# Optimization experiments

Hardware: AMD Instinct MI355X
Metric: run time of the kernel (lower is better)

The kernel has to match this reference:

```python
import jax, jax.numpy as jnp
import numpy as np

B, TQ, TK = 4, 256, 256
Q, K, H = 256, 256, 256


def setup_inputs() -> dict:
    key = jax.random.key(0)
    ks = jax.random.split(key, 10)
    s = 0.05
    return {
        "queries": jax.random.normal(ks[0], (B, TQ, Q), dtype=jnp.float32),
        "keys": jax.random.normal(ks[1], (B, TK, K), dtype=jnp.float32),
        # lengths in [T//2, T] so no fully-masked query rows (torch would NaN there too)
        "query_lengths": jax.random.randint(ks[2], (B,), TQ // 2, TQ + 1),
        "key_lengths": jax.random.randint(ks[3], (B,), TK // 2, TK + 1),
        # nn.Linear(Q+K, H): weight applied as x @ W1; torch concat order is [keys, queries]
        "W1": jax.random.normal(ks[4], (K + Q, H), dtype=jnp.float32) * s,
        "b1": jax.random.normal(ks[5], (H,), dtype=jnp.float32) * s,
        "W2": jax.random.normal(ks[6], (H, H), dtype=jnp.float32) * s,
        "b2": jax.random.normal(ks[7], (H,), dtype=jnp.float32) * s,
        "W3": jax.random.normal(ks[8], (H, 1), dtype=jnp.float32) * s,
        "b3": jax.random.normal(ks[9], (1,), dtype=jnp.float32) * s,
    }


def reference(queries, keys, query_lengths, key_lengths, W1, b1, W2, b2, W3, b3):
    Bn, Tq, Qd = queries.shape
    Tk, Kd = keys.shape[1], keys.shape[2]
    # Split the first linear: concat([keys, queries]) @ W1 == keys@W1[:K] + queries@W1[K:]
    kh = jnp.einsum("bkd,dh->bkh", keys, W1[:Kd])      # [B,Tk,H]
    qh = jnp.einsum("bqd,dh->bqh", queries, W1[Kd:])   # [B,Tq,H]
    h = jax.nn.relu(qh[:, :, None, :] + kh[:, None, :, :] + b1)  # [B,Tq,Tk,H]
    h = jax.nn.relu(jnp.einsum("bqkh,hg->bqkg", h, W2) + b2)     # [B,Tq,Tk,H]
    scores = jnp.einsum("bqkh,h->bqk", h, W3[:, 0]) + b3[0]       # [B,Tq,Tk]
    # mask True where position is padding (query OR key out of range)
    mask = (jnp.arange(Tq)[None, :, None] >= query_lengths[:, None, None]) | (
        jnp.arange(Tk)[None, None, :] >= key_lengths[:, None, None]
    )
    scores = jnp.where(mask, -1e30, scores)
    probs = jax.nn.softmax(scores, axis=-1)
    probs = jnp.where(mask, 0.0, probs)
    return jnp.einsum("bqk,bkd->bqd", probs, keys)  # [B,Tq,K]
```

## Files before the change

### kernel.cpp

```cpp
#include <hip/hip_runtime.h>
#include <cstdint>

#define BATCH 4
#define TQ 256
#define TK 256
#define DIM 256
#define HD 256

typedef _Float16 f16x8 __attribute__((ext_vector_type(8)));
typedef float f32x4 __attribute__((ext_vector_type(4)));

union U4H8 { uint4 u; f16x8 v; };

#define KEEP(x) asm volatile("" : "+v"(x))

__device__ __forceinline__ unsigned short f2h(float f) {
    _Float16 h = (_Float16)f;
    unsigned short u;
    __builtin_memcpy(&u, &h, 2);
    return u;
}

__device__ __forceinline__ uint32_t pk2h(float a, float b) {
    auto r = __builtin_amdgcn_cvt_pkrtz(a, b);
    uint32_t w;
    __builtin_memcpy(&w, &r, 4);
    return w;
}

__global__ __launch_bounds__(256) void prep_all(
    const float* __restrict__ queries, const float* __restrict__ keys,
    const float* __restrict__ W1, const float* __restrict__ b1,
    const float* __restrict__ W2,
    float* __restrict__ qh, float* __restrict__ kh,
    unsigned short* __restrict__ W2T) {
    int i = blockIdx.x;
    int t = threadIdx.x;
    if (i >= 512) {
        __shared__ float tile[32][33];
        int bi = i - 512;
        int tx = t & 31, ty = t >> 5;
        int tc = (bi & 7) * 32, tn = (bi >> 3) * 32;
#pragma unroll
        for (int r = 0; r < 4; ++r)
            tile[ty + r * 8][tx] = W2[(tc + ty + r * 8) * HD + tn + tx];
        __syncthreads();
#pragma unroll
        for (int r = 0; r < 4; ++r)
            W2T[(tn + ty + r * 8) * HD + tc + tx] = f2h(tile[tx][ty + r * 8]);
        return;
    }
    bool isQ = i < 256;
    int r0 = (i & 255) * 4;
    const float* X = isQ ? queries : keys;
    const float* W = W1 + (isQ ? DIM * HD : 0);
    float* O = isQ ? qh : kh;
    __shared__ float xs[4][DIM];
#pragma unroll
    for (int r = 0; r < 4; ++r) xs[r][t] = X[(r0 + r) * DIM + t];
    __syncthreads();
    float acc[4] = {0.f, 0.f, 0.f, 0.f};
#pragma unroll 8
    for (int d = 0; d < DIM; ++d) {
        float w = W[d * HD + t];
#pragma unroll
        for (int r = 0; r < 4; ++r) acc[r] = fmaf(xs[r][d], w, acc[r]);
    }
    float bias = isQ ? b1[t] : 0.f;
#pragma unroll
    for (int r = 0; r < 4; ++r) O[(r0 + r) * HD + t] = acc[r] + bias;
}

__global__ __launch_bounds__(256, 2) void mlp_attn(
    const float* __restrict__ qh, const float* __restrict__ kh,
    const unsigned short* __restrict__ W2T,
    const float* __restrict__ b2, const float* __restrict__ W3,
    const float* __restrict__ keys,
    const int* __restrict__ qlens, const int* __restrict__ klens,
    float* __restrict__ out) {
    int orig = blockIdx.x;
    int bid = ((orig & 7) << 6) | (orig >> 3);
    int b = bid >> 7;
    int q0 = (bid & 127) << 1;
    int t = threadIdx.x;
    int qlen = qlens[b];
    float* orow = out + (b * TQ + q0) * DIM;
    if (q0 >= qlen) { orow[t] = 0.f; orow[DIM + t] = 0.f; return; }
    bool v1 = (q0 + 1) < qlen;
    int klen = klens[b];
    int nch = (klen + 31) >> 5;

    __shared__ uint4 Afrag[2][8][4][64];
    __shared__ float sprt[4][2][TK];
    __shared__ float srow[2][TK];
    __shared__ float red[16];

    int w = t >> 6, lane = t & 63;
    int col = lane & 15, quad = lane >> 4;

    int nb = w << 6;
    uint4 bfr[4][8];
    float b2v[4], w3v[4];
#pragma unroll
    for (int nt = 0; nt < 4; ++nt) {
        int n = nb + (nt << 4) + col;
        const uint4* r = (const uint4*)(W2T + n * HD) + quad;
#pragma unroll
        for (int s = 0; s < 8; ++s) bfr[nt][s] = r[s * 4];
        b2v[nt] = b2[n];
        w3v[nt] = W3[n];
    }

    int rsub = ((w & 1) << 4) | col;
    const float* qrow = qh + (b * TQ + q0 + (w >> 1)) * HD + (quad << 3);
    const float* kbase = kh + b * TK * HD + (quad << 3);

    auto stage = [&](int c, int d) {
        const float* krow = kbase + ((c << 5) + rsub) * HD;
        uint4* as = &Afrag[d][0][w][lane];
#pragma unroll
        for (int s = 0; s < 8; ++s) {
            const float4 k0 = *(const float4*)(krow + s * 32);
            const float4 k1 = *(const float4*)(krow + s * 32 + 4);
            const float4 qa = *(const float4*)(qrow + s * 32);
            const float4 qb = *(const float4*)(qrow + s * 32 + 4);
            uint4 wv;
            wv.x = pk2h(fmaxf(k0.x + qa.x, 0.f), fmaxf(k0.y + qa.y, 0.f));
            wv.y = pk2h(fmaxf(k0.z + qa.z, 0.f), fmaxf(k0.w + qa.w, 0.f));
            wv.z = pk2h(fmaxf(k1.x + qb.x, 0.f), fmaxf(k1.y + qb.y, 0.f));
            wv.w = pk2h(fmaxf(k1.z + qb.z, 0.f), fmaxf(k1.w + qb.w, 0.f));
            as[s * 256] = wv;
        }
    };

    stage(0, 0);

#pragma unroll
    for (int nt = 0; nt < 4; ++nt)
#pragma unroll
        for (int s = 0; s < 8; ++s) {
            KEEP(bfr[nt][s].x); KEEP(bfr[nt][s].y);
            KEEP(bfr[nt][s].z); KEEP(bfr[nt][s].w);
        }

    __syncthreads();

    for (int c = 0; c < nch; ++c) {
        int cur = c & 1;
        if (c + 1 < nch) stage(c + 1, cur ^ 1);

#pragma unroll
        for (int hf = 0; hf < 2; ++hf) {
            f32x4 acc[2][4] = {};
#pragma unroll
            for (int s = 0; s < 8; ++s) {
#pragma unroll
                for (int m2 = 0; m2 < 2; ++m2) {
                    U4H8 au;
                    au.u = Afrag[cur][s][(hf << 1) | m2][lane];
#pragma unroll
                    for (int nt = 0; nt < 4; ++nt) {
                        U4H8 bu;
                        bu.u = bfr[nt][s];
                        acc[m2][nt] = __builtin_amdgcn_mfma_f32_16x16x32_f16(
                            au.v, bu.v, acc[m2][nt], 0, 0, 0);
                    }
                }
            }
#pragma unroll
            for (int m2 = 0; m2 < 2; ++m2) {
                float part[4];
#pragma unroll
                for (int r = 0; r < 4; ++r) {
                    float pa = 0.f;
#pragma unroll
                    for (int nt = 0; nt < 4; ++nt)
                        pa = fmaf(fmaxf(acc[m2][nt][r] + b2v[nt], 0.f), w3v[nt], pa);
                    part[r] = pa;
                }
#pragma unroll
                for (int off = 1; off < 16; off <<= 1)
#pragma unroll
                    for (int r = 0; r < 4; ++r)
                        part[r] += __shfl_xor(part[r], off, 64);
                if (col == 0) {
                    float4 p4 = make_float4(part[0], part[1], part[2], part[3]);
                    *(float4*)&sprt[w][hf][(c << 5) | (m2 << 4) | (quad << 2)] = p4;
                }
            }
        }
        __syncthreads();
    }

    float s0 = -3.4e38f, s1 = -3.4e38f;
    if (t < klen) {
        s0 = (sprt[0][0][t] + sprt[1][0][t]) + (sprt[2][0][t] + sprt[3][0][t]);
        s1 = (sprt[0][1][t] + sprt[1][1][t]) + (sprt[2][1][t] + sprt[3][1][t]);
    }
    float m0 = s0, m1 = s1;
#pragma unroll
    for (int off = 1; off < 64; off <<= 1) {
        m0 = fmaxf(m0, __shfl_xor(m0, off, 64));
        m1 = fmaxf(m1, __shfl_xor(m1, off, 64));
    }
    if (lane == 0) { red[w] = m0; red[8 + w] = m1; }
    __syncthreads();
    m0 = fmaxf(fmaxf(red[0], red[1]), fmaxf(red[2], red[3]));
    m1 = fmaxf(fmaxf(red[8], red[9]), fmaxf(red[10], red[11]));
    float e0 = (t < klen) ? __expf(s0 - m0) : 0.f;
    float e1 = (t < klen) ? __expf(s1 - m1) : 0.f;
    float u0 = e0, u1 = e1;
#pragma unroll
    for (int off = 1; off < 64; off <<= 1) {
        u0 += __shfl_xor(u0, off, 64);
        u1 += __shfl_xor(u1, off, 64);
    }
    if (lane == 0) { red[4 + w] = u0; red[12 + w] = u1; }
    __syncthreads();
    float d0 = red[4] + red[5] + red[6] + red[7];
    float d1 = red[12] + red[13] + red[14] + red[15];
    srow[0][t] = e0 / d0;
    srow[1][t] = e1 / d1;
    __syncthreads();

    float a0 = 0.f, a1 = 0.f;
    const float* kp = keys + b * TK * DIM + t;
#pragma unroll 8
    for (int k = 0; k < klen; ++k) {
        float v = kp[k * DIM];
        a0 = fmaf(srow[0][k], v, a0);
        a1 = fmaf(srow[1][k], v, a1);
    }
    orow[t] = a0;
    orow[DIM + t] = v1 ? a1 : 0.f;
}

extern "C" void kernel_launch(void* const* d_in, const int* in_sizes, int n_in,
                              void* d_out, int out_size, void* d_ws, size_t ws_size,
                              hipStream_t stream) {
    (void)in_sizes; (void)n_in; (void)out_size; (void)ws_size;
    const float* queries = (const float*)d_in[0];
    const float* keys    = (const float*)d_in[1];
    const int*   qlens   = (const int*)d_in[2];
    const int*   klens   = (const int*)d_in[3];
    const float* W1      = (const float*)d_in[4];
    const float* b1      = (const float*)d_in[5];
    const float* W2      = (const float*)d_in[6];
    const float* b2      = (const float*)d_in[7];
    const float* W3      = (const float*)d_in[8];
    float* out = (float*)d_out;

    float* qh = (float*)d_ws;
    float* kh = qh + BATCH * TQ * HD;
    unsigned short* W2T = (unsigned short*)(kh + BATCH * TK * HD);

    prep_all<<<576, 256, 0, stream>>>(queries, keys, W1, b1, W2, qh, kh, W2T);
    mlp_attn<<<BATCH * TQ / 2, 256, 0, stream>>>(
        qh, kh, W2T, b2, W3, keys, qlens, klens, out);
}
```

Baseline: 146.0 us.

## Double mlp_attn block to 512 threads, splitting N tiles across eight waves

The main kernel now runs 8 waves per block instead of 4. Each wave holds half as many W2 column tiles in registers, and staging of the relu(q+k) fragments is split across wave pairs. Per-wave partial scores are now accumulated with shared-memory atomics instead of a 4-way partial buffer. The softmax and the final probs@keys pass are remapped so each of the 512 threads handles one row element and uses float4 key loads with a 4-way k split plus shuffle reduction. The aim is lower register pressure and more latency hiding, at the cost of LDS atomics and non-deterministic summation order. The probs@keys loop now always runs to 256 and relies on probabilities being zeroed past klen.

Result: slower. 172.7 us (+18.3%).

```diff
diff --git a/kernel.cpp b/kernel.cpp
--- a/kernel.cpp
+++ b/kernel.cpp
@@ -71,7 +71,7 @@
     for (int r = 0; r < 4; ++r) O[(r0 + r) * HD + t] = acc[r] + bias;
 }
 
-__global__ __launch_bounds__(256, 2) void mlp_attn(
+__global__ __launch_bounds__(512, 4) void mlp_attn(
     const float* __restrict__ qh, const float* __restrict__ kh,
     const unsigned short* __restrict__ W2T,
     const float* __restrict__ b2, const float* __restrict__ W3,
@@ -85,25 +85,23 @@
     int t = threadIdx.x;
     int qlen = qlens[b];
     float* orow = out + (b * TQ + q0) * DIM;
-    if (q0 >= qlen) { orow[t] = 0.f; orow[DIM + t] = 0.f; return; }
+    if (q0 >= qlen) { orow[t] = 0.f; return; }
     bool v1 = (q0 + 1) < qlen;
     int klen = klens[b];
     int nch = (klen + 31) >> 5;
 
     __shared__ uint4 Afrag[2][8][4][64];
-    __shared__ float sprt[4][2][TK];
     __shared__ float srow[2][TK];
     __shared__ float red[16];
 
     int w = t >> 6, lane = t & 63;
     int col = lane & 15, quad = lane >> 4;
 
-    int nb = w << 6;
-    uint4 bfr[4][8];
-    float b2v[4], w3v[4];
-#pragma unroll
-    for (int nt = 0; nt < 4; ++nt) {
-        int n = nb + (nt << 4) + col;
+    uint4 bfr[2][8];
+    float b2v[2], w3v[2];
+#pragma unroll
+    for (int nt = 0; nt < 2; ++nt) {
+        int n = (w << 5) + (nt << 4) + col;
         const uint4* r = (const uint4*)(W2T + n * HD) + quad;
 #pragma unroll
         for (int s = 0; s < 8; ++s) bfr[nt][s] = r[s * 4];
@@ -111,32 +109,34 @@
         w3v[nt] = W3[n];
     }
 
-    int rsub = ((w & 1) << 4) | col;
-    const float* qrow = qh + (b * TQ + q0 + (w >> 1)) * HD + (quad << 3);
-    const float* kbase = kh + b * TK * HD + (quad << 3);
+    int mt = w >> 1;
+    int sbase = (w & 1) << 2;
+    const float* qrow = qh + (b * TQ + q0 + (mt >> 1)) * HD + (quad << 3) + sbase * 32;
+    const float* kbase = kh + (b * TK + ((mt & 1) << 4) + col) * HD + (quad << 3) + sbase * 32;
 
     auto stage = [&](int c, int d) {
-        const float* krow = kbase + ((c << 5) + rsub) * HD;
-        uint4* as = &Afrag[d][0][w][lane];
-#pragma unroll
-        for (int s = 0; s < 8; ++s) {
-            const float4 k0 = *(const float4*)(krow + s * 32);
-            const float4 k1 = *(const float4*)(krow + s * 32 + 4);
-            const float4 qa = *(const float4*)(qrow + s * 32);
-            const float4 qb = *(const float4*)(qrow + s * 32 + 4);
+        const float* krow = kbase + ((c << 5)) * HD;
+        uint4* as = &Afrag[d][sbase][mt][lane];
+#pragma unroll 2
+        for (int j = 0; j < 4; ++j) {
+            const float4 k0 = *(const float4*)(krow + j * 32);
+            const float4 k1 = *(const float4*)(krow + j * 32 + 4);
+            const float4 qa = *(const float4*)(qrow + j * 32);
+            const float4 qb = *(const float4*)(qrow + j * 32 + 4);
             uint4 wv;
             wv.x = pk2h(fmaxf(k0.x + qa.x, 0.f), fmaxf(k0.y + qa.y, 0.f));
             wv.y = pk2h(fmaxf(k0.z + qa.z, 0.f), fmaxf(k0.w + qa.w, 0.f));
             wv.z = pk2h(fmaxf(k1.x + qb.x, 0.f), fmaxf(k1.y + qb.y, 0.f));
             wv.w = pk2h(fmaxf(k1.z + qb.z, 0.f), fmaxf(k1.w + qb.w, 0.f));
-            as[s * 256] = wv;
+            as[j * 256] = wv;
         }
     };
 
     stage(0, 0);
-
-#pragma unroll
-    for (int nt = 0; nt < 4; ++nt)
+    ((float*)srow)[t] = 0.f;
+
+#pragma unroll
+    for (int nt = 0; nt < 2; ++nt)
 #pragma unroll
         for (int s = 0; s < 8; ++s) {
             KEEP(bfr[nt][s].x); KEEP(bfr[nt][s].y);
@@ -151,7 +151,7 @@
 
 #pragma unroll
         for (int hf = 0; hf < 2; ++hf) {
-            f32x4 acc[2][4] = {};
+            f32x4 acc[2][2] = {};
 #pragma unroll
             for (int s = 0; s < 8; ++s) {
 #pragma unroll
@@ -159,7 +159,7 @@
                     U4H8 au;
                     au.u = Afrag[cur][s][(hf << 1) | m2][lane];
 #pragma unroll
-                    for (int nt = 0; nt < 4; ++nt) {
+                    for (int nt = 0; nt < 2; ++nt) {
                         U4H8 bu;
                         bu.u = bfr[nt][s];
                         acc[m2][nt] = __builtin_amdgcn_mfma_f32_16x16x32_f16(
@@ -172,67 +172,73 @@
                 float part[4];
 #pragma unroll
                 for (int r = 0; r < 4; ++r) {
-                    float pa = 0.f;
-#pragma unroll
-                    for (int nt = 0; nt < 4; ++nt)
-                        pa = fmaf(fmaxf(acc[m2][nt][r] + b2v[nt], 0.f), w3v[nt], pa);
-                    part[r] = pa;
+                    float pa = fmaxf(acc[m2][1][r] + b2v[1], 0.f) * w3v[1];
+                    part[r] = fmaf(fmaxf(acc[m2][0][r] + b2v[0], 0.f), w3v[0], pa);
                 }
 #pragma unroll
                 for (int off = 1; off < 16; off <<= 1)
 #pragma unroll
                     for (int r = 0; r < 4; ++r)
                         part[r] += __shfl_xor(part[r], off, 64);
-                if (col == 0) {
-                    float4 p4 = make_float4(part[0], part[1], part[2], part[3]);
-                    *(float4*)&sprt[w][hf][(c << 5) | (m2 << 4) | (quad << 2)] = p4;
-                }
+                if (col == 0)
+#pragma unroll
+                    for (int r = 0; r < 4; ++r)
+                        atomicAdd(&srow[hf][(c << 5) | (m2 << 4) | (quad << 2) | r],
+                                  part[r]);
             }
         }
         __syncthreads();
     }
 
-    float s0 = -3.4e38f, s1 = -3.4e38f;
-    if (t < klen) {
-        s0 = (sprt[0][0][t] + sprt[1][0][t]) + (sprt[2][0][t] + sprt[3][0][t]);
-        s1 = (sprt[0][1][t] + sprt[1][1][t]) + (sprt[2][1][t] + sprt[3][1][t]);
-    }
-    float m0 = s0, m1 = s1;
-#pragma unroll
-    for (int off = 1; off < 64; off <<= 1) {
-        m0 = fmaxf(m0, __shfl_xor(m0, off, 64));
-        m1 = fmaxf(m1, __shfl_xor(m1, off, 64));
-    }
-    if (lane == 0) { red[w] = m0; red[8 + w] = m1; }
-    __syncthreads();
-    m0 = fmaxf(fmaxf(red[0], red[1]), fmaxf(red[2], red[3]));
-    m1 = fmaxf(fmaxf(red[8], red[9]), fmaxf(red[10], red[11]));
-    float e0 = (t < klen) ? __expf(s0 - m0) : 0.f;
-    float e1 = (t < klen) ? __expf(s1 - m1) : 0.f;
-    float u0 = e0, u1 = e1;
-#pragma unroll
-    for (int off = 1; off < 64; off <<= 1) {
-        u0 += __shfl_xor(u0, off, 64);
-        u1 += __shfl_xor(u1, off, 64);
-    }
-    if (lane == 0) { red[4 + w] = u0; red[12 + w] = u1; }
-    __syncthreads();
-    float d0 = red[4] + red[5] + red[6] + red[7];
-    float d1 = red[12] + red[13] + red[14] + red[15];
-    srow[0][t] = e0 / d0;
-    srow[1][t] = e1 / d1;
-    __syncthreads();
-
-    float a0 = 0.f, a1 = 0.f;
-    const float* kp = keys + b * TK * DIM + t;
+    int rr = t >> 8, kk = t & 255;
+    float s = (kk < klen) ? srow[rr][kk] : -3.4e38f;
+    float m = s;
+#pragma unroll
+    for (int off = 1; off < 64; off <<= 1) m = fmaxf(m, __shfl_xor(m, off, 64));
+    if (lane == 0) red[w] = m;
+    __syncthreads();
+    {
+        int rb = rr << 2;
+        m = fmaxf(fmaxf(red[rb], red[rb + 1]), fmaxf(red[rb + 2], red[rb + 3]));
+    }
+    float e = (kk < klen) ? __expf(s - m) : 0.f;
+    float u = e;
+#pragma unroll
+    for (int off = 1; off < 64; off <<= 1) u += __shfl_xor(u, off, 64);
+    if (lane == 0) red[8 + w] = u;
+    __syncthreads();
+    float denom;
+    {
+        int rb = (rr << 2) + 8;
+        denom = (red[rb] + red[rb + 1]) + (red[rb + 2] + red[rb + 3]);
+    }
+    srow[rr][kk] = e / denom;
+    __syncthreads();
+
+    int cq = (t & 255) >> 2, ks = t & 3;
+    const float* kp = keys + b * TK * DIM + (cq << 2);
+    float4 a = make_float4(0.f, 0.f, 0.f, 0.f);
 #pragma unroll 8
-    for (int k = 0; k < klen; ++k) {
-        float v = kp[k * DIM];
-        a0 = fmaf(srow[0][k], v, a0);
-        a1 = fmaf(srow[1][k], v, a1);
-    }
-    orow[t] = a0;
-    orow[DIM + t] = v1 ? a1 : 0.f;
+    for (int i = 0; i < 64; ++i) {
+        int k = (i << 2) | ks;
+        float p = srow[rr][k];
+        const float4 kv = *(const float4*)(kp + k * DIM);
+        a.x = fmaf(p, kv.x, a.x);
+        a.y = fmaf(p, kv.y, a.y);
+        a.z = fmaf(p, kv.z, a.z);
+        a.w = fmaf(p, kv.w, a.w);
+    }
+#pragma unroll
+    for (int off = 1; off <= 2; off <<= 1) {
+        a.x += __shfl_xor(a.x, off, 64);
+        a.y += __shfl_xor(a.y, off, 64);
+        a.z += __shfl_xor(a.z, off, 64);
+        a.w += __shfl_xor(a.w, off, 64);
+    }
+    if (ks == 0) {
+        float4 o = (rr == 1 && !v1) ? make_float4(0.f, 0.f, 0.f, 0.f) : a;
+        *(float4*)(orow + rr * DIM + (cq << 2)) = o;
+    }
 }
 
 extern "C" void kernel_launch(void* const* d_in, const int* in_sizes, int n_in,
@@ -255,6 +261,6 @@
     unsigned short* W2T = (unsigned short*)(kh + BATCH * TK * HD);
 
     prep_all<<<576, 256, 0, stream>>>(queries, keys, W1, b1, W2, qh, kh, W2T);
-    mlp_attn<<<BATCH * TQ / 2, 256, 0, stream>>>(
+    mlp_attn<<<BATCH * TQ / 2, 512, 0, stream>>>(
         qh, kh, W2T, b2, W3, keys, qlens, klens, out);
 }
```

## Interleave next-chunk kh loads and staging with MFMA tiles, cache q rows in LDS

Applied to the files above, without the earlier changes.

The per-chunk loop is restructured so that the global kh loads and the A-fragment staging for the next chunk are split into pieces. These pieces are interleaved between the MFMA m-tiles and epilogues, with sched_barriers fixing the order. Query hidden rows are copied once into LDS and read from there instead of from global memory on every stage. The aim is to hide global load latency behind matrix work, at the cost of more live registers and smaller accumulator tiles, which may reduce MFMA batching.

New measurement: 134.7 us. 7.7% less time.

```diff
diff --git a/kernel.cpp b/kernel.cpp
--- a/kernel.cpp
+++ b/kernel.cpp
@@ -93,6 +93,7 @@
     __shared__ uint4 Afrag[2][8][4][64];
     __shared__ float sprt[4][2][TK];
     __shared__ float srow[2][TK];
+    __shared__ float Qlds[2][HD];
     __shared__ float red[16];
 
     int w = t >> 6, lane = t & 63;
@@ -111,19 +112,20 @@
         w3v[nt] = W3[n];
     }
 
+    int qsel = w >> 1;
     int rsub = ((w & 1) << 4) | col;
-    const float* qrow = qh + (b * TQ + q0 + (w >> 1)) * HD + (quad << 3);
-    const float* kbase = kh + b * TK * HD + (quad << 3);
-
-    auto stage = [&](int c, int d) {
-        const float* krow = kbase + ((c << 5) + rsub) * HD;
-        uint4* as = &Afrag[d][0][w][lane];
+    const float* kbase = kh + (b * TK + rsub) * HD + (quad << 3);
+
+    {
+        const float* qrowg = qh + (b * TQ + q0 + qsel) * HD + (quad << 3);
+        const float* krow = kbase;
+        uint4* as = &Afrag[0][0][w][lane];
 #pragma unroll
         for (int s = 0; s < 8; ++s) {
             const float4 k0 = *(const float4*)(krow + s * 32);
             const float4 k1 = *(const float4*)(krow + s * 32 + 4);
-            const float4 qa = *(const float4*)(qrow + s * 32);
-            const float4 qb = *(const float4*)(qrow + s * 32 + 4);
+            const float4 qa = *(const float4*)(qrowg + s * 32);
+            const float4 qb = *(const float4*)(qrowg + s * 32 + 4);
             uint4 wv;
             wv.x = pk2h(fmaxf(k0.x + qa.x, 0.f), fmaxf(k0.y + qa.y, 0.f));
             wv.y = pk2h(fmaxf(k0.z + qa.z, 0.f), fmaxf(k0.w + qa.w, 0.f));
@@ -131,9 +133,9 @@
             wv.w = pk2h(fmaxf(k1.z + qb.z, 0.f), fmaxf(k1.w + qb.w, 0.f));
             as[s * 256] = wv;
         }
-    };
-
-    stage(0, 0);
+    }
+    Qlds[0][t] = qh[(b * TQ + q0) * HD + t];
+    Qlds[1][t] = qh[(b * TQ + q0 + 1) * HD + t];
 
 #pragma unroll
     for (int nt = 0; nt < 4; ++nt)
@@ -145,49 +147,103 @@
 
     __syncthreads();
 
+    auto sloop = [&](int cur, int mt, f32x4* acc) {
+#pragma unroll
+        for (int s = 0; s < 8; ++s) {
+            U4H8 au;
+            au.u = Afrag[cur][s][mt][lane];
+#pragma unroll
+            for (int nt = 0; nt < 4; ++nt) {
+                U4H8 bu;
+                bu.u = bfr[nt][s];
+                acc[nt] = __builtin_amdgcn_mfma_f32_16x16x32_f16(
+                    au.v, bu.v, acc[nt], 0, 0, 0);
+            }
+        }
+    };
+    auto epi = [&](int c, int mt, const f32x4* acc) {
+        int hf = mt >> 1, m2 = mt & 1;
+        float part[4];
+#pragma unroll
+        for (int r = 0; r < 4; ++r) {
+            float pa = 0.f;
+#pragma unroll
+            for (int nt = 0; nt < 4; ++nt)
+                pa = fmaf(fmaxf(acc[nt][r] + b2v[nt], 0.f), w3v[nt], pa);
+            part[r] = pa;
+        }
+#pragma unroll
+        for (int off = 1; off < 16; off <<= 1)
+#pragma unroll
+            for (int r = 0; r < 4; ++r)
+                part[r] += __shfl_xor(part[r], off, 64);
+        if (col == 0)
+            *(float4*)&sprt[w][hf][(c << 5) | (m2 << 4) | (quad << 2)] =
+                make_float4(part[0], part[1], part[2], part[3]);
+    };
+
     for (int c = 0; c < nch; ++c) {
         int cur = c & 1;
-        if (c + 1 < nch) stage(c + 1, cur ^ 1);
-
-#pragma unroll
-        for (int hf = 0; hf < 2; ++hf) {
-            f32x4 acc[2][4] = {};
-#pragma unroll
-            for (int s = 0; s < 8; ++s) {
-#pragma unroll
-                for (int m2 = 0; m2 < 2; ++m2) {
-                    U4H8 au;
-                    au.u = Afrag[cur][s][(hf << 1) | m2][lane];
-#pragma unroll
-                    for (int nt = 0; nt < 4; ++nt) {
-                        U4H8 bu;
-                        bu.u = bfr[nt][s];
-                        acc[m2][nt] = __builtin_amdgcn_mfma_f32_16x16x32_f16(
-                            au.v, bu.v, acc[m2][nt], 0, 0, 0);
-                    }
-                }
+        bool stg = (c + 1 < nch);
+        const float* krow = kbase + (((c + 1) << 5)) * HD;
+        uint4* as1 = &Afrag[cur ^ 1][0][w][lane];
+
+        auto wslot = [&](int s, const float4& k0, const float4& k1) {
+            const float4 qa = *(const float4*)&Qlds[qsel][s * 32 + (quad << 3)];
+            const float4 qb = *(const float4*)&Qlds[qsel][s * 32 + (quad << 3) + 4];
+            uint4 wv;
+            wv.x = pk2h(fmaxf(k0.x + qa.x, 0.f), fmaxf(k0.y + qa.y, 0.f));
+            wv.y = pk2h(fmaxf(k0.z + qa.z, 0.f), fmaxf(k0.w + qa.w, 0.f));
+            wv.z = pk2h(fmaxf(k1.x + qb.x, 0.f), fmaxf(k1.y + qb.y, 0.f));
+            wv.w = pk2h(fmaxf(k1.z + qb.z, 0.f), fmaxf(k1.w + qb.w, 0.f));
+            as1[s * 256] = wv;
+        };
+
+        float4 A0, A1, A2, A3, B0, B1, B2, B3;
+        if (stg) {
+            A0 = *(const float4*)(krow);       A1 = *(const float4*)(krow + 4);
+            A2 = *(const float4*)(krow + 32);  A3 = *(const float4*)(krow + 36);
+        }
+        __builtin_amdgcn_sched_barrier(0);
+
+        {
+            f32x4 acc[4] = {};
+            sloop(cur, 0, acc);
+            if (stg) {
+                wslot(0, A0, A1); wslot(1, A2, A3);
+                B0 = *(const float4*)(krow + 64);  B1 = *(const float4*)(krow + 68);
+                B2 = *(const float4*)(krow + 96);  B3 = *(const float4*)(krow + 100);
             }
-#pragma unroll
-            for (int m2 = 0; m2 < 2; ++m2) {
-                float part[4];
-#pragma unroll
-                for (int r = 0; r < 4; ++r) {
-                    float pa = 0.f;
-#pragma unroll
-                    for (int nt = 0; nt < 4; ++nt)
-                        pa = fmaf(fmaxf(acc[m2][nt][r] + b2v[nt], 0.f), w3v[nt], pa);
-                    part[r] = pa;
-                }
-#pragma unroll
-                for (int off = 1; off < 16; off <<= 1)
-#pragma unroll
-                    for (int r = 0; r < 4; ++r)
-                        part[r] += __shfl_xor(part[r], off, 64);
-                if (col == 0) {
-                    float4 p4 = make_float4(part[0], part[1], part[2], part[3]);
-                    *(float4*)&sprt[w][hf][(c << 5) | (m2 << 4) | (quad << 2)] = p4;
-                }
+            __builtin_amdgcn_sched_barrier(0);
+            epi(c, 0, acc);
+            if (stg) {
+                wslot(2, B0, B1); wslot(3, B2, B3);
+                A0 = *(const float4*)(krow + 128); A1 = *(const float4*)(krow + 132);
+                A2 = *(const float4*)(krow + 160); A3 = *(const float4*)(krow + 164);
             }
+            __builtin_amdgcn_sched_barrier(0);
+        }
+        {
+            f32x4 acc[4] = {};
+            sloop(cur, 1, acc);
+            if (stg) {
+                wslot(4, A0, A1); wslot(5, A2, A3);
+                B0 = *(const float4*)(krow + 192); B1 = *(const float4*)(krow + 196);
+                B2 = *(const float4*)(krow + 224); B3 = *(const float4*)(krow + 228);
+            }
+            __builtin_amdgcn_sched_barrier(0);
+            epi(c, 1, acc);
+            if (stg) { wslot(6, B0, B1); wslot(7, B2, B3); }
+        }
+        {
+            f32x4 acc[4] = {};
+            sloop(cur, 2, acc);
+            epi(c, 2, acc);
+        }
+        {
+            f32x4 acc[4] = {};
+            sloop(cur, 3, acc);
+            epi(c, 3, acc);
         }
         __syncthreads();
     }
```

## Store fp16 projections, stage key tiles via direct LDS loads, 4 queries per block

Applied to the files above, without the earlier changes.

The prep kernel now writes qh and kh as fp16, with an XOR swizzle applied to the kh rows. The main kernel uses 512-thread blocks that each handle 4 query rows and 64-key chunks. Key tiles are streamed into LDS with global_load_lds, and the fp16 add+ReLU is done in registers right before the MFMA, with W2 fragments held as the A operand. This cuts global traffic for kh and reuses each key tile across 4 queries, but it needs more LDS, uses fp16 accumulation for the hidden pre-activation, and adds s_setprio hints.

Result: slower. 149.4 us (+2.4%).

```diff
diff --git a/kernel.cpp b/kernel.cpp
--- a/kernel.cpp
+++ b/kernel.cpp
@@ -21,18 +21,22 @@
     return u;
 }
 
-__device__ __forceinline__ uint32_t pk2h(float a, float b) {
-    auto r = __builtin_amdgcn_cvt_pkrtz(a, b);
-    uint32_t w;
-    __builtin_memcpy(&w, &r, 4);
-    return w;
+__device__ __forceinline__ f16x8 relu8(f16x8 h) {
+    f16x8 z = {};
+#if __has_builtin(__builtin_elementwise_max)
+    return __builtin_elementwise_max(h, z);
+#else
+#pragma unroll
+    for (int i = 0; i < 8; ++i) h[i] = h[i] > (_Float16)0 ? h[i] : (_Float16)0;
+    return h;
+#endif
 }
 
 __global__ __launch_bounds__(256) void prep_all(
     const float* __restrict__ queries, const float* __restrict__ keys,
     const float* __restrict__ W1, const float* __restrict__ b1,
     const float* __restrict__ W2,
-    float* __restrict__ qh, float* __restrict__ kh,
+    unsigned short* __restrict__ qhh, unsigned short* __restrict__ khh,
     unsigned short* __restrict__ W2T) {
     int i = blockIdx.x;
     int t = threadIdx.x;
@@ -54,7 +58,6 @@
     int r0 = (i & 255) * 4;
     const float* X = isQ ? queries : keys;
     const float* W = W1 + (isQ ? DIM * HD : 0);
-    float* O = isQ ? qh : kh;
     __shared__ float xs[4][DIM];
 #pragma unroll
     for (int r = 0; r < 4; ++r) xs[r][t] = X[(r0 + r) * DIM + t];
@@ -66,81 +69,85 @@
 #pragma unroll
         for (int r = 0; r < 4; ++r) acc[r] = fmaf(xs[r][d], w, acc[r]);
     }
-    float bias = isQ ? b1[t] : 0.f;
-#pragma unroll
-    for (int r = 0; r < 4; ++r) O[(r0 + r) * HD + t] = acc[r] + bias;
-}
-
-__global__ __launch_bounds__(256, 2) void mlp_attn(
-    const float* __restrict__ qh, const float* __restrict__ kh,
+    if (isQ) {
+        float bias = b1[t];
+#pragma unroll
+        for (int r = 0; r < 4; ++r) qhh[(r0 + r) * HD + t] = f2h(acc[r] + bias);
+    } else {
+#pragma unroll
+        for (int r = 0; r < 4; ++r) {
+            int rr = r0 + r;
+            khh[rr * HD + (t ^ ((rr & 7) << 3))] = f2h(acc[r]);
+        }
+    }
+}
+
+__global__ __launch_bounds__(512, 2) void mlp_attn(
+    const unsigned short* __restrict__ khh,
+    const unsigned short* __restrict__ qhh,
     const unsigned short* __restrict__ W2T,
     const float* __restrict__ b2, const float* __restrict__ W3,
     const float* __restrict__ keys,
     const int* __restrict__ qlens, const int* __restrict__ klens,
     float* __restrict__ out) {
     int orig = blockIdx.x;
-    int bid = ((orig & 7) << 6) | (orig >> 3);
-    int b = bid >> 7;
-    int q0 = (bid & 127) << 1;
+    int bid = ((orig & 7) << 5) | (orig >> 3);
+    int b = bid >> 6;
+    int q0 = (bid & 63) << 2;
     int t = threadIdx.x;
     int qlen = qlens[b];
-    float* orow = out + (b * TQ + q0) * DIM;
-    if (q0 >= qlen) { orow[t] = 0.f; orow[DIM + t] = 0.f; return; }
-    bool v1 = (q0 + 1) < qlen;
+    float* obase = out + (b * TQ + q0) * DIM;
+    if (q0 >= qlen) { obase[t] = 0.f; obase[512 + t] = 0.f; return; }
     int klen = klens[b];
-    int nch = (klen + 31) >> 5;
-
-    __shared__ uint4 Afrag[2][8][4][64];
-    __shared__ float sprt[4][2][TK];
-    __shared__ float srow[2][TK];
-    __shared__ float red[16];
+    int nch = (klen + 63) >> 6;
+
+    __shared__ unsigned short khbuf[2][64 * HD];
+    __shared__ unsigned short qbuf[4][HD];
+    __shared__ float sprt[8][4][TK];
+    __shared__ float pbuf[4][TK];
+    __shared__ float red[32];
 
     int w = t >> 6, lane = t & 63;
     int col = lane & 15, quad = lane >> 4;
 
-    int nb = w << 6;
-    uint4 bfr[4][8];
-    float b2v[4], w3v[4];
-#pragma unroll
-    for (int nt = 0; nt < 4; ++nt) {
-        int n = nb + (nt << 4) + col;
+    auto stage = [&](int c, int d) {
+        const char* src = (const char*)(khh + ((size_t)b * TK + (c << 6)) * HD) + t * 16;
+        char* dst = (char*)&khbuf[d][0] + t * 16;
+#pragma unroll
+        for (int i = 0; i < 4; ++i)
+            __builtin_amdgcn_global_load_lds((const uint32_t*)(src + i * 8192),
+                                             (uint32_t*)(dst + i * 8192), 16, 0, 0);
+    };
+    stage(0, 0);
+
+    uint4 afr[2][8];
+#pragma unroll
+    for (int nt = 0; nt < 2; ++nt) {
+        int n = (w << 5) + (nt << 4) + col;
         const uint4* r = (const uint4*)(W2T + n * HD) + quad;
 #pragma unroll
-        for (int s = 0; s < 8; ++s) bfr[nt][s] = r[s * 4];
-        b2v[nt] = b2[n];
-        w3v[nt] = W3[n];
-    }
-
-    int rsub = ((w & 1) << 4) | col;
-    const float* qrow = qh + (b * TQ + q0 + (w >> 1)) * HD + (quad << 3);
-    const float* kbase = kh + b * TK * HD + (quad << 3);
-
-    auto stage = [&](int c, int d) {
-        const float* krow = kbase + ((c << 5) + rsub) * HD;
-        uint4* as = &Afrag[d][0][w][lane];
+        for (int s = 0; s < 8; ++s) afr[nt][s] = r[s * 4];
+    }
+    float b2v[2][4], w3v[2][4];
+#pragma unroll
+    for (int nt = 0; nt < 2; ++nt)
+#pragma unroll
+        for (int r = 0; r < 4; ++r) {
+            int n = (w << 5) + (nt << 4) + (quad << 2) + r;
+            b2v[nt][r] = b2[n];
+            w3v[nt][r] = W3[n];
+        }
+
+    if (t < 128)
+        *(uint4*)((char*)&qbuf[0][0] + t * 16) =
+            *(const uint4*)((const char*)(qhh + ((size_t)b * TQ + q0) * HD) + t * 16);
+
+#pragma unroll
+    for (int nt = 0; nt < 2; ++nt)
 #pragma unroll
         for (int s = 0; s < 8; ++s) {
-            const float4 k0 = *(const float4*)(krow + s * 32);
-            const float4 k1 = *(const float4*)(krow + s * 32 + 4);
-            const float4 qa = *(const float4*)(qrow + s * 32);
-            const float4 qb = *(const float4*)(qrow + s * 32 + 4);
-            uint4 wv;
-            wv.x = pk2h(fmaxf(k0.x + qa.x, 0.f), fmaxf(k0.y + qa.y, 0.f));
-            wv.y = pk2h(fmaxf(k0.z + qa.z, 0.f), fmaxf(k0.w + qa.w, 0.f));
-            wv.z = pk2h(fmaxf(k1.x + qb.x, 0.f), fmaxf(k1.y + qb.y, 0.f));
-            wv.w = pk2h(fmaxf(k1.z + qb.z, 0.f), fmaxf(k1.w + qb.w, 0.f));
-            as[s * 256] = wv;
-        }
-    };
-
-    stage(0, 0);
-
-#pragma unroll
-    for (int nt = 0; nt < 4; ++nt)
-#pragma unroll
-        for (int s = 0; s < 8; ++s) {
-            KEEP(bfr[nt][s].x); KEEP(bfr[nt][s].y);
-            KEEP(bfr[nt][s].z); KEEP(bfr[nt][s].w);
+            KEEP(afr[nt][s].x); KEEP(afr[nt][s].y);
+            KEEP(afr[nt][s].z); KEEP(afr[nt][s].w);
         }
 
     __syncthreads();
@@ -148,91 +155,99 @@
     for (int c = 0; c < nch; ++c) {
         int cur = c & 1;
         if (c + 1 < nch) stage(c + 1, cur ^ 1);
-
-#pragma unroll
-        for (int hf = 0; hf < 2; ++hf) {
-            f32x4 acc[2][4] = {};
-#pragma unroll
-            for (int s = 0; s < 8; ++s) {
-#pragma unroll
-                for (int m2 = 0; m2 < 2; ++m2) {
-                    U4H8 au;
-                    au.u = Afrag[cur][s][(hf << 1) | m2][lane];
-#pragma unroll
-                    for (int nt = 0; nt < 4; ++nt) {
-                        U4H8 bu;
-                        bu.u = bfr[nt][s];
-                        acc[m2][nt] = __builtin_amdgcn_mfma_f32_16x16x32_f16(
-                            au.v, bu.v, acc[m2][nt], 0, 0, 0);
-                    }
+        const unsigned short* kb = &khbuf[cur][0];
+
+#pragma unroll
+        for (int q = 0; q < 4; ++q) {
+            U4H8 qf[8];
+#pragma unroll
+            for (int s = 0; s < 8; ++s)
+                qf[s].u = *(const uint4*)&qbuf[q][(s << 5) + (quad << 3)];
+#pragma unroll
+            for (int kg = 0; kg < 4; ++kg) {
+                int row = (kg << 4) | col;
+                const unsigned short* kr = kb + row * HD;
+                int sw = (row & 7) << 3;
+                f32x4 acc0 = {}, acc1 = {};
+                __builtin_amdgcn_s_setprio(1);
+#pragma unroll
+                for (int s = 0; s < 8; ++s) {
+                    int el = (((s << 5) | (quad << 3)) ^ sw);
+                    U4H8 kf;
+                    kf.u = *(const uint4*)(kr + el);
+                    f16x8 h = relu8(kf.v + qf[s].v);
+                    U4H8 a0, a1;
+                    a0.u = afr[0][s];
+                    a1.u = afr[1][s];
+                    acc0 = __builtin_amdgcn_mfma_f32_16x16x32_f16(a0.v, h, acc0, 0, 0, 0);
+                    acc1 = __builtin_amdgcn_mfma_f32_16x16x32_f16(a1.v, h, acc1, 0, 0, 0);
                 }
+                __builtin_amdgcn_s_setprio(0);
+                float part = 0.f;
+#pragma unroll
+                for (int r = 0; r < 4; ++r) {
+                    part = fmaf(fmaxf(acc0[r] + b2v[0][r], 0.f), w3v[0][r], part);
+                    part = fmaf(fmaxf(acc1[r] + b2v[1][r], 0.f), w3v[1][r], part);
+                }
+                part += __shfl_xor(part, 16, 64);
+                part += __shfl_xor(part, 32, 64);
+                if (quad == 0)
+                    sprt[w][q][(c << 6) | (kg << 4) | col] = part;
             }
-#pragma unroll
-            for (int m2 = 0; m2 < 2; ++m2) {
-                float part[4];
-#pragma unroll
-                for (int r = 0; r < 4; ++r) {
-                    float pa = 0.f;
-#pragma unroll
-                    for (int nt = 0; nt < 4; ++nt)
-                        pa = fmaf(fmaxf(acc[m2][nt][r] + b2v[nt], 0.f), w3v[nt], pa);
-                    part[r] = pa;
-                }
-#pragma unroll
-                for (int off = 1; off < 16; off <<= 1)
-#pragma unroll
-                    for (int r = 0; r < 4; ++r)
-                        part[r] += __shfl_xor(part[r], off, 64);
-                if (col == 0) {
-                    float4 p4 = make_float4(part[0], part[1], part[2], part[3]);
-                    *(float4*)&sprt[w][hf][(c << 5) | (m2 << 4) | (quad << 2)] = p4;
-                }
-            }
         }
         __syncthreads();
     }
 
-    float s0 = -3.4e38f, s1 = -3.4e38f;
-    if (t < klen) {
-        s0 = (sprt[0][0][t] + sprt[1][0][t]) + (sprt[2][0][t] + sprt[3][0][t]);
-        s1 = (sprt[0][1][t] + sprt[1][1][t]) + (sprt[2][1][t] + sprt[3][1][t]);
-    }
-    float m0 = s0, m1 = s1;
+    int g = t >> 8, kk = t & 255, wg = w & 3;
+    int r2 = g << 1;
+    float sc0 = 0.f, sc1 = 0.f;
+#pragma unroll
+    for (int wv = 0; wv < 8; ++wv) {
+        sc0 += sprt[wv][r2][kk];
+        sc1 += sprt[wv][r2 | 1][kk];
+    }
+    if (kk >= klen) { sc0 = -3.4e38f; sc1 = -3.4e38f; }
+    float m0 = sc0, m1 = sc1;
 #pragma unroll
     for (int off = 1; off < 64; off <<= 1) {
         m0 = fmaxf(m0, __shfl_xor(m0, off, 64));
         m1 = fmaxf(m1, __shfl_xor(m1, off, 64));
     }
-    if (lane == 0) { red[w] = m0; red[8 + w] = m1; }
-    __syncthreads();
-    m0 = fmaxf(fmaxf(red[0], red[1]), fmaxf(red[2], red[3]));
-    m1 = fmaxf(fmaxf(red[8], red[9]), fmaxf(red[10], red[11]));
-    float e0 = (t < klen) ? __expf(s0 - m0) : 0.f;
-    float e1 = (t < klen) ? __expf(s1 - m1) : 0.f;
+    if (lane == 0) { red[(g << 3) | wg] = m0; red[(g << 3) | 4 | wg] = m1; }
+    __syncthreads();
+    m0 = fmaxf(fmaxf(red[(g << 3)], red[(g << 3) | 1]),
+               fmaxf(red[(g << 3) | 2], red[(g << 3) | 3]));
+    m1 = fmaxf(fmaxf(red[(g << 3) | 4], red[(g << 3) | 5]),
+               fmaxf(red[(g << 3) | 6], red[(g << 3) | 7]));
+    float e0 = (kk < klen) ? __expf(sc0 - m0) : 0.f;
+    float e1 = (kk < klen) ? __expf(sc1 - m1) : 0.f;
     float u0 = e0, u1 = e1;
 #pragma unroll
     for (int off = 1; off < 64; off <<= 1) {
         u0 += __shfl_xor(u0, off, 64);
         u1 += __shfl_xor(u1, off, 64);
     }
-    if (lane == 0) { red[4 + w] = u0; red[12 + w] = u1; }
-    __syncthreads();
-    float d0 = red[4] + red[5] + red[6] + red[7];
-    float d1 = red[12] + red[13] + red[14] + red[15];
-    srow[0][t] = e0 / d0;
-    srow[1][t] = e1 / d1;
-    __syncthreads();
-
+    if (lane == 0) { red[16 | (g << 3) | wg] = u0; red[16 | (g << 3) | 4 | wg] = u1; }
+    __syncthreads();
+    float d0 = (red[16 | (g << 3)] + red[16 | (g << 3) | 1]) +
+               (red[16 | (g << 3) | 2] + red[16 | (g << 3) | 3]);
+    float d1 = (red[16 | (g << 3) | 4] + red[16 | (g << 3) | 5]) +
+               (red[16 | (g << 3) | 6] + red[16 | (g << 3) | 7]);
+    pbuf[r2][kk] = e0 / d0;
+    pbuf[r2 | 1][kk] = e1 / d1;
+    __syncthreads();
+
+    const float* kp = keys + b * TK * DIM + kk;
     float a0 = 0.f, a1 = 0.f;
-    const float* kp = keys + b * TK * DIM + t;
 #pragma unroll 8
     for (int k = 0; k < klen; ++k) {
         float v = kp[k * DIM];
-        a0 = fmaf(srow[0][k], v, a0);
-        a1 = fmaf(srow[1][k], v, a1);
-    }
-    orow[t] = a0;
-    orow[DIM + t] = v1 ? a1 : 0.f;
+        a0 = fmaf(pbuf[r2][k], v, a0);
+        a1 = fmaf(pbuf[r2 | 1][k], v, a1);
+    }
+    float* orow = obase + r2 * DIM;
+    orow[kk] = (q0 + r2 < qlen) ? a0 : 0.f;
+    orow[DIM + kk] = (q0 + r2 + 1 < qlen) ? a1 : 0.f;
 }
 
 extern "C" void kernel_launch(void* const* d_in, const int* in_sizes, int n_in,
@@ -250,11 +265,11 @@
     const float* W3      = (const float*)d_in[8];
     float* out = (float*)d_out;
 
-    float* qh = (float*)d_ws;
-    float* kh = qh + BATCH * TQ * HD;
-    unsigned short* W2T = (unsigned short*)(kh + BATCH * TK * HD);
-
-    prep_all<<<576, 256, 0, stream>>>(queries, keys, W1, b1, W2, qh, kh, W2T);
-    mlp_attn<<<BATCH * TQ / 2, 256, 0, stream>>>(
-        qh, kh, W2T, b2, W3, keys, qlens, klens, out);
-}
+    unsigned short* qhh = (unsigned short*)d_ws;
+    unsigned short* khh = qhh + BATCH * TQ * HD;
+    unsigned short* W2T = khh + BATCH * TK * HD;
+
+    prep_all<<<576, 256, 0, stream>>>(queries, keys, W1, b1, W2, qhh, khh, W2T);
+    mlp_attn<<<256, 512, 0, stream>>>(
+        khh, qhh, W2T, b2, W3, keys, qlens, klens, out);
+}
```
